# Performance work log

Measured on AMD Instinct MI355X. Metric: run time of the kernel, lower is better.

## Reference

```python
import jax, jax.numpy as jnp
import numpy as np
import math

EMBED_DIM = 128
NUM_HEADS = 16
HEAD_DIM = EMBED_DIM // NUM_HEADS  # = 8 = n_wires of the quantum circuit


def setup_inputs() -> dict:
    key = jax.random.key(0)
    k1, k2, k3 = jax.random.split(key, 3)
    B, S = 4, 2048
    x = jax.random.normal(k1, (B, S, EMBED_DIM), dtype=jnp.float32)
    # shared trainable RX angles of the single q_layer (applied to every head)
    theta = jax.random.normal(k2, (HEAD_DIM,), dtype=jnp.float32)
    w_out = jax.random.normal(k3, (EMBED_DIM, EMBED_DIM), dtype=jnp.float32) / math.sqrt(EMBED_DIM)
    mask = jnp.ones((B, S), dtype=jnp.int32)
    return {"x": x, "theta": theta, "w_out": w_out, "mask": mask}


def quantum_linear(x_head, theta):
    # Circuit: RX(x_i) encode + RX(theta_i) on wire i, CNOT chain (i, i+1),
    # then <Z_j>. For product state |psi_i> = RX(phi_i)|0>, <Z_i> = cos(phi_i),
    # and the CNOT chain gives final <Z_j> = prod_{i<=j} cos(phi_i).
    phi = x_head + theta  # [..., D] broadcast over leading dims
    return jnp.cumprod(jnp.cos(phi), axis=-1)


def reference(x, theta, w_out, mask):
    B, S, E = x.shape
    H, D = NUM_HEADS, HEAD_DIM
    xs = x.reshape(B, S, H, D)
    q = quantum_linear(xs, theta).transpose(0, 2, 1, 3)  # [B, H, S, D]; k = v = q
    scores = jnp.einsum("bhsd,bhtd->bhst", q, q) / math.sqrt(D)
    scores = jnp.where(mask[:, None, None, :] == 0, -1e9, scores)
    probs = jax.nn.softmax(scores, axis=-1)  # dropout is identity in eval
    attn = jnp.einsum("bhst,bhtd->bhsd", probs, q)
    attn = attn.transpose(0, 2, 1, 3).reshape(B, S, E)
    return attn @ w_out.T
```

## Files before the change

kernel.cpp:

```cpp
#include <hip/hip_runtime.h>
#include <hip/hip_bf16.h>
#include <hip/hip_fp16.h>

#define NB 4
#define NS 2048
#define NE 128
#define NH 16
#define ND 8

typedef __attribute__((ext_vector_type(8))) _Float16 half8;
typedef __attribute__((ext_vector_type(4))) float f32x4;

#define VSTRIDEH 1032

__device__ __forceinline__ unsigned int pkrtz(float a, float b) {
    typedef __fp16 fp16v2 __attribute__((ext_vector_type(2)));
    union { fp16v2 h; unsigned int u; } v;
    v.h = __builtin_amdgcn_cvt_pkrtz(a, b);
    return v.u;
}
__device__ __forceinline__ unsigned short f2h(float a) {
    return __half_as_ushort(__float2half(a));
}
__device__ __forceinline__ half8 mk_half8(unsigned u0, unsigned u1,
                                          unsigned u2, unsigned u3) {
    union { half8 h; unsigned u[4]; } v;
    v.u[0] = u0; v.u[1] = u1; v.u[2] = u2; v.u[3] = u3;
    return v.h;
}
__device__ __forceinline__ void qrow(const float* xp, const float* th, float* p) {
    float4 a = *(const float4*)xp, c = *(const float4*)(xp + 4);
    float t = 1.f;
    t *= cosf(a.x + th[0]); p[0] = t; t *= cosf(a.y + th[1]); p[1] = t;
    t *= cosf(a.z + th[2]); p[2] = t; t *= cosf(a.w + th[3]); p[3] = t;
    t *= cosf(c.x + th[4]); p[4] = t; t *= cosf(c.y + th[5]); p[5] = t;
    t *= cosf(c.z + th[6]); p[6] = t; t *= cosf(c.w + th[7]); p[7] = t;
}

__global__ __launch_bounds__(512, 8) void attn_kernel(
        const float* __restrict__ x,
        const float* __restrict__ theta,
        const int* __restrict__ mask,
        unsigned short* __restrict__ mid) {
    __shared__ unsigned short qt[1024 * ND + 24];
    __shared__ unsigned short vTh[9 * VSTRIDEH];
    __shared__ unsigned short qm[256 * ND + 8];

    const int bid = blockIdx.x;
    const int bh = bid >> 3;
    const int b = bh >> 4, h = bh & (NH - 1);
    const int meighth = bid & 7;
    const int tid = threadIdx.x;

    const float SC = 0.71421629f;

    float th[ND];
#pragma unroll
    for (int d = 0; d < ND; d++) th[d] = theta[d];

    if (tid < 256) {
        int m = meighth * 256 + tid;
        float pm[ND];
        qrow(x + ((size_t)(b * NS + m) * NE + h * ND), th, pm);
        uint4 qa;
        qa.x = pkrtz(pm[0] * SC, pm[1] * SC);
        qa.y = pkrtz(pm[2] * SC, pm[3] * SC);
        qa.z = pkrtz(pm[4] * SC, pm[5] * SC);
        qa.w = pkrtz(pm[6] * SC, pm[7] * SC);
        *(uint4*)&qm[tid * ND] = qa;
    }
    if (tid < 24) qt[1024 * ND + tid] = 0;

    const int wave = tid >> 6, lane = tid & 63;
    const int quad = lane >> 4, l15 = lane & 15;
    const int vrow = (l15 < 9) ? l15 : 8;
    const unsigned short* vbase = &vTh[vrow * VSTRIDEH];
    half8 hz = {0, 0, 0, 0, 0, 0, 0, 0};

    const int chs = tid >> 4, si = tid & 15;
    const int ta = 4 * (si >> 2) + 2 * (si & 1) + 16 * ((si >> 1) & 1);
    const int r0l = chs * 32 + ta;

    f32x4 O0 = {0.f, 0.f, 0.f, 0.f}, O1 = {0.f, 0.f, 0.f, 0.f};

    for (int p = 0; p < 2; p++) {
        if (p) __syncthreads();
        {
            int t0 = p * 1024 + r0l, t1 = t0 + 1;
            float p0[ND], p1[ND];
            qrow(x + ((size_t)(b * NS + t0) * NE + h * ND), th, p0);
            qrow(x + ((size_t)(b * NS + t1) * NE + h * ND), th, p1);
            float sk0 = mask[b * NS + t0] ? SC : 0.f;
            float sk1 = mask[b * NS + t1] ? SC : 0.f;
            uint4 qa, qb;
            qa.x = pkrtz(p0[0] * SC, p0[1] * SC);
            qa.y = pkrtz(p0[2] * SC, p0[3] * SC);
            qa.z = pkrtz(p0[4] * SC, p0[5] * SC);
            qa.w = pkrtz(p0[6] * SC, p0[7] * SC);
            qb.x = pkrtz(p1[0] * SC, p1[1] * SC);
            qb.y = pkrtz(p1[2] * SC, p1[3] * SC);
            qb.z = pkrtz(p1[4] * SC, p1[5] * SC);
            qb.w = pkrtz(p1[6] * SC, p1[7] * SC);
            *(uint4*)&qt[r0l * ND]       = qa;
            *(uint4*)&qt[(r0l + 1) * ND] = qb;
#pragma unroll
            for (int d = 0; d < ND; d++)
                *(unsigned int*)&vTh[d * VSTRIDEH + chs * 32 + 2 * si] =
                    pkrtz(p0[d] * sk0, p1[d] * sk1);
            *(unsigned int*)&vTh[8 * VSTRIDEH + chs * 32 + 2 * si] = pkrtz(sk0, sk1);
        }
        __syncthreads();

        half8 bm0 = quad ? hz : *(const half8*)&qm[(wave * 32 + l15) * ND];
        half8 bm1 = quad ? hz : *(const half8*)&qm[(wave * 32 + 16 + l15) * ND];

        for (int ch = 0; ch < 32; ch++) {
            int tbl = ch * 32;
            half8 at0 = *(const half8*)&qt[(tbl + l15) * ND + quad * 8];
            half8 at1 = *(const half8*)&qt[(tbl + 16 + l15) * ND + quad * 8];
            half8 vf  = *(const half8*)&vbase[tbl + quad * 8];
            f32x4 z = {0.f, 0.f, 0.f, 0.f};

            f32x4 s00 = __builtin_amdgcn_mfma_f32_16x16x32_f16(at0, bm0, z, 0, 0, 0);
            f32x4 s01 = __builtin_amdgcn_mfma_f32_16x16x32_f16(at0, bm1, z, 0, 0, 0);
            f32x4 s10 = __builtin_amdgcn_mfma_f32_16x16x32_f16(at1, bm0, z, 0, 0, 0);
            f32x4 s11 = __builtin_amdgcn_mfma_f32_16x16x32_f16(at1, bm1, z, 0, 0, 0);

            half8 pA0 = mk_half8(
                pkrtz(__builtin_amdgcn_exp2f(s00[0]), __builtin_amdgcn_exp2f(s00[1])),
                pkrtz(__builtin_amdgcn_exp2f(s00[2]), __builtin_amdgcn_exp2f(s00[3])),
                pkrtz(__builtin_amdgcn_exp2f(s10[0]), __builtin_amdgcn_exp2f(s10[1])),
                pkrtz(__builtin_amdgcn_exp2f(s10[2]), __builtin_amdgcn_exp2f(s10[3])));
            half8 pA1 = mk_half8(
                pkrtz(__builtin_amdgcn_exp2f(s01[0]), __builtin_amdgcn_exp2f(s01[1])),
                pkrtz(__builtin_amdgcn_exp2f(s01[2]), __builtin_amdgcn_exp2f(s01[3])),
                pkrtz(__builtin_amdgcn_exp2f(s11[0]), __builtin_amdgcn_exp2f(s11[1])),
                pkrtz(__builtin_amdgcn_exp2f(s11[2]), __builtin_amdgcn_exp2f(s11[3])));

            O0 = __builtin_amdgcn_mfma_f32_16x16x32_f16(pA0, vf, O0, 0, 0, 0);
            O1 = __builtin_amdgcn_mfma_f32_16x16x32_f16(pA1, vf, O1, 0, 0, 0);
        }
    }

    const int mbase = meighth * 256 + wave * 32;
#pragma unroll
    for (int mt = 0; mt < 2; mt++) {
        f32x4 O = mt ? O1 : O0;
#pragma unroll
        for (int r = 0; r < 4; r++) {
            float lsum = __shfl(O[r], (lane & 48) | 8, 64);
            float v = O[r] / lsum;
            if (l15 < ND) {
                int m = mbase + mt * 16 + quad * 4 + r;
                mid[(size_t)(b * NS + m) * NE + h * ND + l15] = f2h(v);
            }
        }
    }
}

__global__ __launch_bounds__(256) void proj_kernel(
        const unsigned short* __restrict__ mid,
        const float* __restrict__ w,
        float* __restrict__ out) {
    __shared__ unsigned short wf[NE * 136];
    __shared__ unsigned short am[32 * 136];
    const int rb = blockIdx.x * 32;
    const int tid = threadIdx.x;

    for (int i = tid; i < 2048; i += 256) {
        const float* wp = w + i * 8;
        float4 a = *(const float4*)wp, c = *(const float4*)(wp + 4);
        uint4 pk;
        pk.x = pkrtz(a.x, a.y); pk.y = pkrtz(a.z, a.w);
        pk.z = pkrtz(c.x, c.y); pk.w = pkrtz(c.z, c.w);
        int n = i >> 4, k8 = (i & 15) * 8;
        *(uint4*)&wf[n * 136 + k8] = pk;
    }
    for (int i = tid; i < 512; i += 256) {
        int r = i >> 4, k8 = (i & 15) * 8;
        uint4 v = *(const uint4*)&mid[(size_t)(rb + r) * NE + k8];
        *(uint4*)&am[r * 136 + k8] = v;
    }
    __syncthreads();

    const int wave = tid >> 6, lane = tid & 63;
    const int quad = lane >> 4, l15 = lane & 15;
    const int mt = wave & 1, nh = wave >> 1;

    half8 af[4];
#pragma unroll
    for (int kt = 0; kt < 4; kt++)
        af[kt] = *(const half8*)&am[(mt * 16 + l15) * 136 + kt * 32 + quad * 8];

#pragma unroll
    for (int nt = 0; nt < 4; nt++) {
        int n0 = (nh * 4 + nt) * 16;
        f32x4 acc = {0.f, 0.f, 0.f, 0.f};
#pragma unroll
        for (int kt = 0; kt < 4; kt++) {
            half8 bf = *(const half8*)&wf[(n0 + l15) * 136 + kt * 32 + quad * 8];
            acc = __builtin_amdgcn_mfma_f32_16x16x32_f16(af[kt], bf, acc, 0, 0, 0);
        }
#pragma unroll
        for (int r = 0; r < 4; r++)
            out[(size_t)(rb + mt * 16 + quad * 4 + r) * NE + n0 + l15] = acc[r];
    }
}

extern "C" void kernel_launch(void* const* d_in, const int* in_sizes, int n_in,
                              void* d_out, int out_size, void* d_ws, size_t ws_size,
                              hipStream_t stream) {
    const float* x     = (const float*)d_in[0];
    const float* theta = (const float*)d_in[1];
    const float* w_out = (const float*)d_in[2];
    const int*   mask  = (const int*)d_in[3];
    float* out = (float*)d_out;

    unsigned short* mid16 = (unsigned short*)d_ws;

    attn_kernel<<<NB * NH * 8, 512, 0, stream>>>(x, theta, mask, mid16);
    proj_kernel<<<NB * NS / 32, 256, 0, stream>>>(mid16, w_out, out);
}
```

Before: 110.7 us.

## Split attention keys across two blocks and combine partials in projection

Splits the key dimension into two halves handled by separate blocks (grid y=2), each writing unnormalized fp32 partial outputs and row sums to workspace. The projection kernel sums the halves, normalizes, and then does the GEMM. This doubles block count to raise occupancy and parallelism, and drops the intra-block two-pass loop and its barrier. The cost is extra global traffic for the partials. A fallback path keeps a single-block full-sequence kernel with the mask folded in as an additive bias when the workspace is too small. Skipping the max-subtraction in the split is safe only because scores are bounded.

```diff
diff --git a/kernel.cpp b/kernel.cpp
--- a/kernel.cpp
+++ b/kernel.cpp
@@ -11,6 +11,7 @@
 typedef __attribute__((ext_vector_type(8))) _Float16 half8;
 typedef __attribute__((ext_vector_type(4))) float f32x4;
 
+#define VSTRIDE  2056
 #define VSTRIDEH 1032
 
 __device__ __forceinline__ unsigned int pkrtz(float a, float b) {
@@ -37,16 +38,18 @@
     t *= cosf(c.z + th[6]); p[6] = t; t *= cosf(c.w + th[7]); p[7] = t;
 }
 
-__global__ __launch_bounds__(512, 8) void attn_kernel(
+__global__ __launch_bounds__(512) void attn_partial(
         const float* __restrict__ x,
         const float* __restrict__ theta,
         const int* __restrict__ mask,
-        unsigned short* __restrict__ mid) {
+        float* __restrict__ Opart,
+        float* __restrict__ lpart) {
     __shared__ unsigned short qt[1024 * ND + 24];
     __shared__ unsigned short vTh[9 * VSTRIDEH];
     __shared__ unsigned short qm[256 * ND + 8];
 
     const int bid = blockIdx.x;
+    const int half = blockIdx.y;
     const int bh = bid >> 3;
     const int b = bh >> 4, h = bh & (NH - 1);
     const int meighth = bid & 7;
@@ -69,7 +72,35 @@
         qa.w = pkrtz(pm[6] * SC, pm[7] * SC);
         *(uint4*)&qm[tid * ND] = qa;
     }
+    {
+        int chs = tid >> 4, si = tid & 15;
+        int ta = 4 * (si >> 2) + 2 * (si & 1) + 16 * ((si >> 1) & 1);
+        int r0l = chs * 32 + ta;
+        int t0 = half * 1024 + r0l, t1 = t0 + 1;
+        float p0[ND], p1[ND];
+        qrow(x + ((size_t)(b * NS + t0) * NE + h * ND), th, p0);
+        qrow(x + ((size_t)(b * NS + t1) * NE + h * ND), th, p1);
+        float sk0 = mask[b * NS + t0] ? SC : 0.f;
+        float sk1 = mask[b * NS + t1] ? SC : 0.f;
+        uint4 qa, qb;
+        qa.x = pkrtz(p0[0] * SC, p0[1] * SC);
+        qa.y = pkrtz(p0[2] * SC, p0[3] * SC);
+        qa.z = pkrtz(p0[4] * SC, p0[5] * SC);
+        qa.w = pkrtz(p0[6] * SC, p0[7] * SC);
+        qb.x = pkrtz(p1[0] * SC, p1[1] * SC);
+        qb.y = pkrtz(p1[2] * SC, p1[3] * SC);
+        qb.z = pkrtz(p1[4] * SC, p1[5] * SC);
+        qb.w = pkrtz(p1[6] * SC, p1[7] * SC);
+        *(uint4*)&qt[r0l * ND]       = qa;
+        *(uint4*)&qt[(r0l + 1) * ND] = qb;
+#pragma unroll
+        for (int d = 0; d < ND; d++)
+            *(unsigned int*)&vTh[d * VSTRIDEH + chs * 32 + 2 * si] =
+                pkrtz(p0[d] * sk0, p1[d] * sk1);
+        *(unsigned int*)&vTh[8 * VSTRIDEH + chs * 32 + 2 * si] = pkrtz(sk0, sk1);
+    }
     if (tid < 24) qt[1024 * ND + tid] = 0;
+    __syncthreads();
 
     const int wave = tid >> 6, lane = tid & 63;
     const int quad = lane >> 4, l15 = lane & 15;
@@ -77,72 +108,200 @@
     const unsigned short* vbase = &vTh[vrow * VSTRIDEH];
     half8 hz = {0, 0, 0, 0, 0, 0, 0, 0};
 
-    const int chs = tid >> 4, si = tid & 15;
-    const int ta = 4 * (si >> 2) + 2 * (si & 1) + 16 * ((si >> 1) & 1);
-    const int r0l = chs * 32 + ta;
+    half8 bm0 = quad ? hz : *(const half8*)&qm[(wave * 32 + l15) * ND];
+    half8 bm1 = quad ? hz : *(const half8*)&qm[(wave * 32 + 16 + l15) * ND];
 
     f32x4 O0 = {0.f, 0.f, 0.f, 0.f}, O1 = {0.f, 0.f, 0.f, 0.f};
-
-    for (int p = 0; p < 2; p++) {
-        if (p) __syncthreads();
-        {
-            int t0 = p * 1024 + r0l, t1 = t0 + 1;
-            float p0[ND], p1[ND];
-            qrow(x + ((size_t)(b * NS + t0) * NE + h * ND), th, p0);
-            qrow(x + ((size_t)(b * NS + t1) * NE + h * ND), th, p1);
-            float sk0 = mask[b * NS + t0] ? SC : 0.f;
-            float sk1 = mask[b * NS + t1] ? SC : 0.f;
-            uint4 qa, qb;
-            qa.x = pkrtz(p0[0] * SC, p0[1] * SC);
-            qa.y = pkrtz(p0[2] * SC, p0[3] * SC);
-            qa.z = pkrtz(p0[4] * SC, p0[5] * SC);
-            qa.w = pkrtz(p0[6] * SC, p0[7] * SC);
-            qb.x = pkrtz(p1[0] * SC, p1[1] * SC);
-            qb.y = pkrtz(p1[2] * SC, p1[3] * SC);
-            qb.z = pkrtz(p1[4] * SC, p1[5] * SC);
-            qb.w = pkrtz(p1[6] * SC, p1[7] * SC);
-            *(uint4*)&qt[r0l * ND]       = qa;
-            *(uint4*)&qt[(r0l + 1) * ND] = qb;
-#pragma unroll
-            for (int d = 0; d < ND; d++)
-                *(unsigned int*)&vTh[d * VSTRIDEH + chs * 32 + 2 * si] =
-                    pkrtz(p0[d] * sk0, p1[d] * sk1);
-            *(unsigned int*)&vTh[8 * VSTRIDEH + chs * 32 + 2 * si] = pkrtz(sk0, sk1);
+    for (int ch = 0; ch < 32; ch++) {
+        int tbl = ch * 32;
+        half8 at0 = *(const half8*)&qt[(tbl + l15) * ND + quad * 8];
+        half8 at1 = *(const half8*)&qt[(tbl + 16 + l15) * ND + quad * 8];
+        half8 vf  = *(const half8*)&vbase[tbl + quad * 8];
+        f32x4 z = {0.f, 0.f, 0.f, 0.f};
+
+        f32x4 s00 = __builtin_amdgcn_mfma_f32_16x16x32_f16(at0, bm0, z, 0, 0, 0);
+        f32x4 s01 = __builtin_amdgcn_mfma_f32_16x16x32_f16(at0, bm1, z, 0, 0, 0);
+        f32x4 s10 = __builtin_amdgcn_mfma_f32_16x16x32_f16(at1, bm0, z, 0, 0, 0);
+        f32x4 s11 = __builtin_amdgcn_mfma_f32_16x16x32_f16(at1, bm1, z, 0, 0, 0);
+
+        half8 pA0 = mk_half8(
+            pkrtz(__builtin_amdgcn_exp2f(s00[0]), __builtin_amdgcn_exp2f(s00[1])),
+            pkrtz(__builtin_amdgcn_exp2f(s00[2]), __builtin_amdgcn_exp2f(s00[3])),
+            pkrtz(__builtin_amdgcn_exp2f(s10[0]), __builtin_amdgcn_exp2f(s10[1])),
+            pkrtz(__builtin_amdgcn_exp2f(s10[2]), __builtin_amdgcn_exp2f(s10[3])));
+        half8 pA1 = mk_half8(
+            pkrtz(__builtin_amdgcn_exp2f(s01[0]), __builtin_amdgcn_exp2f(s01[1])),
+            pkrtz(__builtin_amdgcn_exp2f(s01[2]), __builtin_amdgcn_exp2f(s01[3])),
+            pkrtz(__builtin_amdgcn_exp2f(s11[0]), __builtin_amdgcn_exp2f(s11[1])),
+            pkrtz(__builtin_amdgcn_exp2f(s11[2]), __builtin_amdgcn_exp2f(s11[3])));
+
+        O0 = __builtin_amdgcn_mfma_f32_16x16x32_f16(pA0, vf, O0, 0, 0, 0);
+        O1 = __builtin_amdgcn_mfma_f32_16x16x32_f16(pA1, vf, O1, 0, 0, 0);
+    }
+
+    const int mbase = meighth * 256 + wave * 32;
+    const size_t pb = ((size_t)half * 64 + bh) * NS;
+#pragma unroll
+    for (int mt = 0; mt < 2; mt++) {
+        f32x4 O = mt ? O1 : O0;
+#pragma unroll
+        for (int r = 0; r < 4; r++) {
+            int m = mbase + mt * 16 + quad * 4 + r;
+            if (l15 < ND)
+                Opart[(pb + m) * ND + l15] = O[r];
+            else if (l15 == ND)
+                lpart[pb + m] = O[r];
         }
-        __syncthreads();
-
-        half8 bm0 = quad ? hz : *(const half8*)&qm[(wave * 32 + l15) * ND];
-        half8 bm1 = quad ? hz : *(const half8*)&qm[(wave * 32 + 16 + l15) * ND];
-
-        for (int ch = 0; ch < 32; ch++) {
-            int tbl = ch * 32;
-            half8 at0 = *(const half8*)&qt[(tbl + l15) * ND + quad * 8];
-            half8 at1 = *(const half8*)&qt[(tbl + 16 + l15) * ND + quad * 8];
-            half8 vf  = *(const half8*)&vbase[tbl + quad * 8];
-            f32x4 z = {0.f, 0.f, 0.f, 0.f};
-
-            f32x4 s00 = __builtin_amdgcn_mfma_f32_16x16x32_f16(at0, bm0, z, 0, 0, 0);
-            f32x4 s01 = __builtin_amdgcn_mfma_f32_16x16x32_f16(at0, bm1, z, 0, 0, 0);
-            f32x4 s10 = __builtin_amdgcn_mfma_f32_16x16x32_f16(at1, bm0, z, 0, 0, 0);
-            f32x4 s11 = __builtin_amdgcn_mfma_f32_16x16x32_f16(at1, bm1, z, 0, 0, 0);
-
-            half8 pA0 = mk_half8(
-                pkrtz(__builtin_amdgcn_exp2f(s00[0]), __builtin_amdgcn_exp2f(s00[1])),
-                pkrtz(__builtin_amdgcn_exp2f(s00[2]), __builtin_amdgcn_exp2f(s00[3])),
-                pkrtz(__builtin_amdgcn_exp2f(s10[0]), __builtin_amdgcn_exp2f(s10[1])),
-                pkrtz(__builtin_amdgcn_exp2f(s10[2]), __builtin_amdgcn_exp2f(s10[3])));
-            half8 pA1 = mk_half8(
-                pkrtz(__builtin_amdgcn_exp2f(s01[0]), __builtin_amdgcn_exp2f(s01[1])),
-                pkrtz(__builtin_amdgcn_exp2f(s01[2]), __builtin_amdgcn_exp2f(s01[3])),
-                pkrtz(__builtin_amdgcn_exp2f(s11[0]), __builtin_amdgcn_exp2f(s11[1])),
-                pkrtz(__builtin_amdgcn_exp2f(s11[2]), __builtin_amdgcn_exp2f(s11[3])));
-
-            O0 = __builtin_amdgcn_mfma_f32_16x16x32_f16(pA0, vf, O0, 0, 0, 0);
-            O1 = __builtin_amdgcn_mfma_f32_16x16x32_f16(pA1, vf, O1, 0, 0, 0);
+    }
+}
+
+__global__ __launch_bounds__(256) void proj_combine(
+        const float* __restrict__ Opart,
+        const float* __restrict__ lpart,
+        const float* __restrict__ w,
+        float* __restrict__ out) {
+    __shared__ unsigned short wf[NE * 136];
+    __shared__ unsigned short am[32 * 136];
+    const int rb = blockIdx.x * 32;
+    const int tid = threadIdx.x;
+
+    for (int i = tid; i < 2048; i += 256) {
+        const float* wp = w + i * 8;
+        float4 a = *(const float4*)wp, c = *(const float4*)(wp + 4);
+        uint4 pk;
+        pk.x = pkrtz(a.x, a.y); pk.y = pkrtz(a.z, a.w);
+        pk.z = pkrtz(c.x, c.y); pk.w = pkrtz(c.z, c.w);
+        int n = i >> 4, k8 = (i & 15) * 8;
+        *(uint4*)&wf[n * 136 + k8] = pk;
+    }
+#pragma unroll
+    for (int k = 0; k < 2; k++) {
+        int c = k * 256 + tid;
+        int r = c >> 4, h = c & 15;
+        int R = rb + r, b = R >> 11, s = R & (NS - 1);
+        size_t row = ((size_t)(b * NH + h)) * NS + s;
+        size_t o0 = row * ND, o1 = o0 + (size_t)64 * NS * ND;
+        float4 a0 = *(const float4*)&Opart[o0];
+        float4 c0 = *(const float4*)&Opart[o0 + 4];
+        float4 a1 = *(const float4*)&Opart[o1];
+        float4 c1 = *(const float4*)&Opart[o1 + 4];
+        float l = lpart[row] + lpart[(size_t)64 * NS + row];
+        float inv = 1.f / l;
+        uint4 pk;
+        pk.x = pkrtz((a0.x + a1.x) * inv, (a0.y + a1.y) * inv);
+        pk.y = pkrtz((a0.z + a1.z) * inv, (a0.w + a1.w) * inv);
+        pk.z = pkrtz((c0.x + c1.x) * inv, (c0.y + c1.y) * inv);
+        pk.w = pkrtz((c0.z + c1.z) * inv, (c0.w + c1.w) * inv);
+        *(uint4*)&am[r * 136 + h * 8] = pk;
+    }
+    __syncthreads();
+
+    const int wave = tid >> 6, lane = tid & 63;
+    const int quad = lane >> 4, l15 = lane & 15;
+    const int mt = wave & 1, nh = wave >> 1;
+
+    half8 af[4];
+#pragma unroll
+    for (int kt = 0; kt < 4; kt++)
+        af[kt] = *(const half8*)&am[(mt * 16 + l15) * 136 + kt * 32 + quad * 8];
+
+#pragma unroll
+    for (int nt = 0; nt < 4; nt++) {
+        int n0 = (nh * 4 + nt) * 16;
+        f32x4 acc = {0.f, 0.f, 0.f, 0.f};
+#pragma unroll
+        for (int kt = 0; kt < 4; kt++) {
+            half8 bf = *(const half8*)&wf[(n0 + l15) * 136 + kt * 32 + quad * 8];
+            acc = __builtin_amdgcn_mfma_f32_16x16x32_f16(af[kt], bf, acc, 0, 0, 0);
         }
-    }
-
+#pragma unroll
+        for (int r = 0; r < 4; r++)
+            out[(size_t)(rb + mt * 16 + quad * 4 + r) * NE + n0 + l15] = acc[r];
+    }
+}
+
+__global__ __launch_bounds__(512) void attn_full(
+        const float* __restrict__ x,
+        const float* __restrict__ theta,
+        const int* __restrict__ mask,
+        unsigned short* __restrict__ mid) {
+    __shared__ unsigned short qhl[NS * ND + 24];
+    __shared__ unsigned short vT[9 * VSTRIDE];
+    __shared__ float kb[NS];
+
+    const int bid = blockIdx.x;
+    const int bh = bid >> 3;
+    const int b = bh >> 4, h = bh & (NH - 1);
+    const int meighth = bid & 7;
+    const int tid = threadIdx.x;
+    const float SC = 0.71421629f;
+
+    float th[ND];
+#pragma unroll
+    for (int d = 0; d < ND; d++) th[d] = theta[d];
+
+    for (int idx = tid; idx < 1024; idx += 512) {
+        int chs = idx >> 4, si = idx & 15;
+        int ta = 4 * (si >> 2) + 2 * (si & 1) + 16 * ((si >> 1) & 1);
+        int r0 = chs * 32 + ta, r1 = r0 + 1;
+        float p0[ND], p1[ND];
+        qrow(x + ((size_t)(b * NS + r0) * NE + h * ND), th, p0);
+        qrow(x + ((size_t)(b * NS + r1) * NE + h * ND), th, p1);
+        uint4 qa, qb;
+        qa.x = pkrtz(p0[0] * SC, p0[1] * SC);
+        qa.y = pkrtz(p0[2] * SC, p0[3] * SC);
+        qa.z = pkrtz(p0[4] * SC, p0[5] * SC);
+        qa.w = pkrtz(p0[6] * SC, p0[7] * SC);
+        qb.x = pkrtz(p1[0] * SC, p1[1] * SC);
+        qb.y = pkrtz(p1[2] * SC, p1[3] * SC);
+        qb.z = pkrtz(p1[4] * SC, p1[5] * SC);
+        qb.w = pkrtz(p1[6] * SC, p1[7] * SC);
+        *(uint4*)&qhl[r0 * ND] = qa;
+        *(uint4*)&qhl[r1 * ND] = qb;
+#pragma unroll
+        for (int d = 0; d < ND; d++)
+            *(unsigned int*)&vT[d * VSTRIDE + chs * 32 + 2 * si] = pkrtz(p0[d], p1[d]);
+        *(unsigned int*)&vT[8 * VSTRIDE + chs * 32 + 2 * si] = 0x3C003C00u;
+    }
+    for (int i = tid; i < NS; i += 512)
+        kb[i] = mask[b * NS + i] ? 0.f : -30000.f;
+    if (tid < 24) qhl[NS * ND + tid] = 0;
+    __syncthreads();
+
+    const int wave = tid >> 6, lane = tid & 63;
+    const int quad = lane >> 4, l15 = lane & 15;
     const int mbase = meighth * 256 + wave * 32;
+    half8 hz = {0, 0, 0, 0, 0, 0, 0, 0};
+    half8 bm0 = quad ? hz : *(const half8*)&qhl[(mbase + l15) * ND];
+    half8 bm1 = quad ? hz : *(const half8*)&qhl[(mbase + 16 + l15) * ND];
+    const int vrow = (l15 < 9) ? l15 : 8;
+    const unsigned short* vbase = &vT[vrow * VSTRIDE];
+
+    f32x4 O0 = {0.f, 0.f, 0.f, 0.f}, O1 = {0.f, 0.f, 0.f, 0.f};
+    for (int ch = 0; ch < 64; ch++) {
+        int tb = ch * 32;
+        half8 at0 = *(const half8*)&qhl[(tb + l15) * ND + quad * 8];
+        half8 at1 = *(const half8*)&qhl[(tb + 16 + l15) * ND + quad * 8];
+        half8 vf  = *(const half8*)&vbase[tb + quad * 8];
+        f32x4 C0 = *(const f32x4*)&kb[tb + quad * 4];
+        f32x4 C1 = *(const f32x4*)&kb[tb + 16 + quad * 4];
+        f32x4 s00 = __builtin_amdgcn_mfma_f32_16x16x32_f16(at0, bm0, C0, 0, 0, 0);
+        f32x4 s01 = __builtin_amdgcn_mfma_f32_16x16x32_f16(at0, bm1, C0, 0, 0, 0);
+        f32x4 s10 = __builtin_amdgcn_mfma_f32_16x16x32_f16(at1, bm0, C1, 0, 0, 0);
+        f32x4 s11 = __builtin_amdgcn_mfma_f32_16x16x32_f16(at1, bm1, C1, 0, 0, 0);
+        half8 pA0 = mk_half8(
+            pkrtz(__builtin_amdgcn_exp2f(s00[0]), __builtin_amdgcn_exp2f(s00[1])),
+            pkrtz(__builtin_amdgcn_exp2f(s00[2]), __builtin_amdgcn_exp2f(s00[3])),
+            pkrtz(__builtin_amdgcn_exp2f(s10[0]), __builtin_amdgcn_exp2f(s10[1])),
+            pkrtz(__builtin_amdgcn_exp2f(s10[2]), __builtin_amdgcn_exp2f(s10[3])));
+        half8 pA1 = mk_half8(
+            pkrtz(__builtin_amdgcn_exp2f(s01[0]), __builtin_amdgcn_exp2f(s01[1])),
+            pkrtz(__builtin_amdgcn_exp2f(s01[2]), __builtin_amdgcn_exp2f(s01[3])),
+            pkrtz(__builtin_amdgcn_exp2f(s11[0]), __builtin_amdgcn_exp2f(s11[1])),
+            pkrtz(__builtin_amdgcn_exp2f(s11[2]), __builtin_amdgcn_exp2f(s11[3])));
+        O0 = __builtin_amdgcn_mfma_f32_16x16x32_f16(pA0, vf, O0, 0, 0, 0);
+        O1 = __builtin_amdgcn_mfma_f32_16x16x32_f16(pA1, vf, O1, 0, 0, 0);
+    }
 #pragma unroll
     for (int mt = 0; mt < 2; mt++) {
         f32x4 O = mt ? O1 : O0;
@@ -158,7 +317,7 @@
     }
 }
 
-__global__ __launch_bounds__(256) void proj_kernel(
+__global__ __launch_bounds__(256) void proj_mid(
         const unsigned short* __restrict__ mid,
         const float* __restrict__ w,
         float* __restrict__ out) {
@@ -166,7 +325,6 @@
     __shared__ unsigned short am[32 * 136];
     const int rb = blockIdx.x * 32;
     const int tid = threadIdx.x;
-
     for (int i = tid; i < 2048; i += 256) {
         const float* wp = w + i * 8;
         float4 a = *(const float4*)wp, c = *(const float4*)(wp + 4);
@@ -182,16 +340,13 @@
         *(uint4*)&am[r * 136 + k8] = v;
     }
     __syncthreads();
-
     const int wave = tid >> 6, lane = tid & 63;
     const int quad = lane >> 4, l15 = lane & 15;
     const int mt = wave & 1, nh = wave >> 1;
-
     half8 af[4];
 #pragma unroll
     for (int kt = 0; kt < 4; kt++)
         af[kt] = *(const half8*)&am[(mt * 16 + l15) * 136 + kt * 32 + quad * 8];
-
 #pragma unroll
     for (int nt = 0; nt < 4; nt++) {
         int n0 = (nh * 4 + nt) * 16;
@@ -216,8 +371,18 @@
     const int*   mask  = (const int*)d_in[3];
     float* out = (float*)d_out;
 
-    unsigned short* mid16 = (unsigned short*)d_ws;
-
-    attn_kernel<<<NB * NH * 8, 512, 0, stream>>>(x, theta, mask, mid16);
-    proj_kernel<<<NB * NS / 32, 256, 0, stream>>>(mid16, w_out, out);
-}
+    const size_t opart_elems = (size_t)2 * 64 * NS * ND;
+    const size_t lpart_elems = (size_t)2 * 64 * NS;
+    const size_t need = (opart_elems + lpart_elems) * sizeof(float);
+
+    if (ws_size >= need) {
+        float* Opart = (float*)d_ws;
+        float* lpart = Opart + opart_elems;
+        attn_partial<<<dim3(NB * NH * 8, 2), 512, 0, stream>>>(x, theta, mask, Opart, lpart);
+        proj_combine<<<NB * NS / 32, 256, 0, stream>>>(Opart, lpart, w_out, out);
+    } else {
+        unsigned short* mid16 = (unsigned short*)d_ws;
+        attn_full<<<NB * NH * 8, 512, 0, stream>>>(x, theta, mask, mid16);
+        proj_mid<<<NB * NS / 32, 256, 0, stream>>>(mid16, w_out, out);
+    }
+}
```

Result: faster. 104.1 us (-6.0%).
